# Kernel optimization log

Measured on AMD Instinct MI355X. Metric: run time of the kernel, lower is better.

## Reference

```python
import jax, jax.numpy as jnp
import numpy as np

B, S, DM, DE, H, DH, DC, DCq, DR = 4, 2048, 1024, 1024, 16, 64, 128, 128, 32
SCALE = 1.0 / np.sqrt(DH + DR)


def _rope_tables(seq_len, dim, theta=10000.0):
    inv = 1.0 / (theta ** (jnp.arange(0, dim, 2, dtype=jnp.float32) / dim))  # [dim/2]
    t = jnp.arange(seq_len, dtype=jnp.float32)
    ang = t[:, None] * inv[None, :]  # [S, dim/2]
    return jnp.cos(ang), jnp.sin(ang)


def _apply_rope(xq, xk, cos, sin):
    # xq, xk: [B, S, H, DR]; complex rotary on (even, odd) pairs
    def rot(x):
        s = x.shape
        xr = x.reshape(*s[:-1], s[-1] // 2, 2)
        r, i = xr[..., 0], xr[..., 1]
        c = cos[None, :s[1], None, :]
        sn = sin[None, :s[1], None, :]
        out = jnp.stack([r * c - i * sn, r * sn + i * c], axis=-1)
        return out.reshape(s)
    return rot(xq), rot(xk)


def setup_inputs() -> dict:
    key = jax.random.key(0)
    ks = jax.random.split(key, 10)
    def lin(k, din, dout):
        return 0.02 * jax.random.normal(k, (din, dout), jnp.float32)
    inp = {
        "x": jax.random.normal(ks[0], (B, S, DM), jnp.float32),
        "mask": jnp.tril(jnp.ones((S, S), jnp.float32))[None, None],
        "W_dkv": lin(ks[1], DM, DC),  "b_dkv": jnp.zeros((DC,), jnp.float32),
        "W_dq":  lin(ks[2], DM, DCq), "b_dq":  jnp.zeros((DCq,), jnp.float32),
        "W_uk":  lin(ks[3], DC, DE),  "b_uk":  jnp.zeros((DE,), jnp.float32),
        "W_uv":  lin(ks[4], DC, DE),  "b_uv":  jnp.zeros((DE,), jnp.float32),
        "W_uq":  lin(ks[5], DCq, DE), "b_uq":  jnp.zeros((DE,), jnp.float32),
        "W_qr":  lin(ks[6], DCq, DR * H), "b_qr": jnp.zeros((DR * H,), jnp.float32),
        "W_kr":  lin(ks[7], DM, DR),  "b_kr": jnp.zeros((DR,), jnp.float32),
        "W_o":   lin(ks[8], DE, DM),  "b_o":  jnp.zeros((DM,), jnp.float32),
    }
    return inp


def reference(x, mask, W_dkv, b_dkv, W_dq, b_dq, W_uk, b_uk, W_uv, b_uv,
              W_uq, b_uq, W_qr, b_qr, W_kr, b_kr, W_o, b_o):
    bs, seq_len, _ = x.shape
    cos, sin = _rope_tables(2 * S, DR)

    c_q = x @ W_dq + b_dq            # [B,S,DCq]
    c_kv = x @ W_dkv + b_dkv         # [B,S,DC]
    k_r = x @ W_kr + b_kr            # [B,S,DR]

    q_c = (c_q @ W_uq + b_uq).reshape(bs, seq_len, H, DH)
    k_c = (c_kv @ W_uk + b_uk).reshape(bs, seq_len, H, DH)
    v_c = (c_kv @ W_uv + b_uv).reshape(bs, seq_len, H, DH)

    q_r = (c_q @ W_qr + b_qr).reshape(bs, seq_len, H, DR)
    k_r = jnp.broadcast_to(k_r[:, :, None, :], (bs, seq_len, H, DR))
    q_r, k_r = _apply_rope(q_r, k_r, cos, sin)

    q_t = jnp.concatenate([q_c, q_r], axis=-1)  # [B,S,H,DH+DR]
    k_t = jnp.concatenate([k_c, k_r], axis=-1)

    attn = jnp.einsum('bqhd,bkhd->bhqk', q_t, k_t) * SCALE  # [B,H,S,S]
    m = jnp.where(mask == 0, -jnp.inf, mask)  # faithful masked_fill then add
    attn = attn + m
    p = jax.nn.softmax(attn, axis=-1)
    out = jnp.einsum('bhqk,bkhd->bqhd', p, v_c).reshape(bs, seq_len, H * DH)
    return out @ W_o + b_o
```

## Files before the change

### kernel.cpp

```cpp
#include <hip/hip_runtime.h>
#include <cstdint>
#include <cstddef>

#define S_ 2048
#define B_ 4
#define H_ 16

typedef __attribute__((ext_vector_type(8))) __bf16 bf16x8;
typedef __attribute__((ext_vector_type(4))) __bf16 bf16x4;
typedef __attribute__((ext_vector_type(4))) float f32x4;
typedef __attribute__((ext_vector_type(16))) float f32x16;

__device__ __forceinline__ f32x4 mfma16(bf16x8 a, bf16x8 b, f32x4 c) {
  return __builtin_amdgcn_mfma_f32_16x16x32_bf16(a, b, c, 0, 0, 0);
}
__device__ __forceinline__ f32x16 mfma32(bf16x8 a, bf16x8 b, f32x16 c) {
  return __builtin_amdgcn_mfma_f32_32x32x16_bf16(a, b, c, 0, 0, 0);
}

__device__ __forceinline__ void gll16(const void* g, void* l) {
  __builtin_amdgcn_global_load_lds(
      (__attribute__((address_space(1))) void*)(uintptr_t)g,
      (__attribute__((address_space(3))) void*)(uint32_t)(uintptr_t)l,
      16, 0, 0);
}

__device__ __forceinline__ int cvtpk(float lo, float hi) {
  int r;
  asm("v_cvt_pk_bf16_f32 %0, %1, %2" : "=v"(r) : "v"(lo), "v"(hi));
  return r;
}

union PAU { int w[4]; bf16x8 v; };

__device__ __forceinline__ bf16x8 packPA(int hi, float a0, float a1, float a2,
                                         float a3, float b0, float b1, float b2,
                                         float b3) {
  const int Ylo = cvtpk(a0, a1);
  const int Yhi = cvtpk(a2, a3);
  const int Xlo = cvtpk(b0, b1);
  const int Xhi = cvtpk(b2, b3);
  const int t0 = __shfl_xor(hi ? Ylo : Xlo, 32);
  const int t1 = __shfl_xor(hi ? Yhi : Xhi, 32);
  PAU u;
  u.w[0] = hi ? t0 : Ylo;
  u.w[1] = hi ? t1 : Yhi;
  u.w[2] = hi ? Xlo : t0;
  u.w[3] = hi ? Xhi : t1;
  return u.v;
}


__global__ __launch_bounds__(256) void mla_cvt_x(const float* __restrict__ x,
                                                 __bf16* __restrict__ xb) {
  const size_t i = ((size_t)blockIdx.x * 256 + threadIdx.x) * 8;
  float4 a = *(const float4*)&x[i];
  float4 b = *(const float4*)&x[i + 4];
  bf16x8 v;
  v[0] = (__bf16)a.x; v[1] = (__bf16)a.y; v[2] = (__bf16)a.z; v[3] = (__bf16)a.w;
  v[4] = (__bf16)b.x; v[5] = (__bf16)b.y; v[6] = (__bf16)b.z; v[7] = (__bf16)b.w;
  *(bf16x8*)&xb[i] = v;
}

__global__ void mla_transpose(const float* __restrict__ W, __bf16* __restrict__ WT,
                              int K, int N) {
  __shared__ float tile[32][33];
  const int n0 = blockIdx.x * 32, k0 = blockIdx.y * 32;
  const int tx = threadIdx.x, ty = threadIdx.y;
#pragma unroll
  for (int i = 0; i < 32; i += 8)
    tile[ty + i][tx] = W[(size_t)(k0 + ty + i) * N + n0 + tx];
  __syncthreads();
#pragma unroll
  for (int i = 0; i < 32; i += 8)
    WT[(size_t)(n0 + ty + i) * K + k0 + tx] = (__bf16)tile[tx][ty + i];
}

__global__ void mla_bias(const float* __restrict__ b_dq, const float* __restrict__ b_dkv,
                         const float* __restrict__ b_kr, const float* __restrict__ b_uq,
                         const float* __restrict__ b_qr, const float* __restrict__ b_uk,
                         const float* __restrict__ b_uv, float* __restrict__ bias_d,
                         float* __restrict__ bias_uq, float* __restrict__ bias_ukv) {
  const int t = blockIdx.x * 256 + threadIdx.x;
  if (t < 384)
    bias_d[t] = (t < 128) ? b_dq[t] : (t < 256) ? b_dkv[t - 128]
               : (t < 288) ? b_kr[t - 256] : 0.f;
  if (t < 1536) bias_uq[t] = (t < 1024) ? b_uq[t] : b_qr[t - 1024];
  if (t < 2048) bias_ukv[t] = (t < 1024) ? b_uk[t] : b_uv[t - 1024];
}

__global__ void mla_rope_tab(float* __restrict__ c, float* __restrict__ sn) {
  const int t = blockIdx.x * 256 + threadIdx.x;
  const int s = t >> 4, i = t & 15;
  const float inv = exp2f(-(float)i * (13.287712379549449f / 16.0f));
  const float ang = (float)s * inv;
  c[t] = cosf(ang);
  sn[t] = sinf(ang);
}

template <bool OUTF32>
__global__ __launch_bounds__(256) void gemm_bf16k(
    const __bf16* __restrict__ A, int lda, const __bf16* __restrict__ BT, int ldbt,
    const float* __restrict__ bias, void* __restrict__ Cout, int ldc, int K) {
  const int n0 = blockIdx.x * 128;
  const int m0 = blockIdx.y * 128;
  const int tid = threadIdx.x;
  const int wave = tid >> 6, lane = tid & 63;
  const int g = lane >> 4, li = lane & 15;
  const int wm = (wave >> 1) * 64, wn = (wave & 1) * 64;
  __shared__ __bf16 __attribute__((aligned(16))) ldsA[128 * 32];
  __shared__ __bf16 __attribute__((aligned(16))) ldsB[128 * 32];

  const f32x4 fz = {0.f, 0.f, 0.f, 0.f};
  f32x4 acc[4][4];
#pragma unroll
  for (int i = 0; i < 4; ++i)
#pragma unroll
    for (int j = 0; j < 4; ++j) acc[i][j] = fz;

  const int srow = lane >> 2;
  const int skc = (lane & 3) * 8;

  for (int k0 = 0; k0 < K; k0 += 32) {
    __syncthreads();
#pragma unroll
    for (int c = 0; c < 4; ++c) {
      const int chunk = wave * 4 + c;
      const int r8 = (chunk & 7) * 16 + srow;
      if (chunk < 8)
        gll16(&A[(size_t)(m0 + r8) * lda + k0 + skc], &ldsA[(chunk & 7) * 512]);
      else
        gll16(&BT[(size_t)(n0 + r8) * ldbt + k0 + skc], &ldsB[(chunk & 7) * 512]);
    }
    __syncthreads();

    bf16x8 af[4], bfv[4];
#pragma unroll
    for (int mi = 0; mi < 4; ++mi)
      af[mi] = *(const bf16x8*)&ldsA[(wm + mi * 16 + li) * 32 + g * 8];
#pragma unroll
    for (int ni = 0; ni < 4; ++ni)
      bfv[ni] = *(const bf16x8*)&ldsB[(wn + ni * 16 + li) * 32 + g * 8];
#pragma unroll
    for (int mi = 0; mi < 4; ++mi)
#pragma unroll
      for (int ni = 0; ni < 4; ++ni)
        acc[mi][ni] = mfma16(af[mi], bfv[ni], acc[mi][ni]);
  }

#pragma unroll
  for (int ni = 0; ni < 4; ++ni) {
    const int col = n0 + wn + ni * 16 + li;
    const float bv = bias[col];
#pragma unroll
    for (int mi = 0; mi < 4; ++mi) {
#pragma unroll
      for (int r = 0; r < 4; ++r) {
        const int row = m0 + wm + mi * 16 + 4 * g + r;
        const float v = acc[mi][ni][r] + bv;
        if (OUTF32)
          ((float*)Cout)[(size_t)row * ldc + col] = v;
        else
          ((__bf16*)Cout)[(size_t)row * ldc + col] = (__bf16)v;
      }
    }
  }
}

#define ALPHA_Q 0.14724394f
__global__ __launch_bounds__(256) void mla_build_qk(
    const __bf16* __restrict__ qup, const __bf16* __restrict__ kvup,
    const __bf16* __restrict__ cqkvr, const float* __restrict__ ropec,
    const float* __restrict__ ropes, __bf16* __restrict__ qt,
    __bf16* __restrict__ ktb) {
  const int bs = blockIdx.x;
  const int b = bs >> 11;
  const int s = bs & 2047;
  __shared__ float krr[32];
  if (threadIdx.x < 16) {
    const int i = threadIdx.x;
    const float r = (float)cqkvr[(size_t)bs * 384 + 256 + 2 * i];
    const float im = (float)cqkvr[(size_t)bs * 384 + 256 + 2 * i + 1];
    const float c = ropec[s * 16 + i], sn = ropes[s * 16 + i];
    krr[2 * i] = r * c - im * sn;
    krr[2 * i + 1] = r * sn + im * c;
  }
  __syncthreads();
  for (int idx = threadIdx.x; idx < 1536; idx += 256) {
    const int h = idx / 96, d = idx - h * 96;
    const size_t orow = ((size_t)(b * H_ + h) * S_ + s) * 96;
    float qv, kv;
    if (d < 64) {
      qv = (float)qup[(size_t)bs * 1536 + h * 64 + d];
      kv = (float)kvup[(size_t)bs * 2048 + h * 64 + d];
    } else {
      const int i = (d - 64) >> 1;
      const float c = ropec[s * 16 + i], sn = ropes[s * 16 + i];
      const float r = (float)qup[(size_t)bs * 1536 + 1024 + h * 32 + 2 * i];
      const float im = (float)qup[(size_t)bs * 1536 + 1024 + h * 32 + 2 * i + 1];
      qv = (((d - 64) & 1) == 0) ? (r * c - im * sn) : (r * sn + im * c);
      kv = krr[d - 64];
    }
    qt[orow + d] = (__bf16)(qv * ALPHA_Q);
    ktb[orow + d] = (__bf16)kv;
  }
}

__global__ __launch_bounds__(256) void mla_vtrans(const __bf16* __restrict__ kvup,
                                                  __bf16* __restrict__ vt) {
  const int s0 = blockIdx.x * 64;
  const int bh = blockIdx.y;
  const int b = bh >> 4, h = bh & 15;
  __shared__ __bf16 __attribute__((aligned(16))) tile[64][72];
  const int t = threadIdx.x;
  {
    const int r = t >> 2, c0 = (t & 3) * 16;
    const size_t src = (size_t)(b * S_ + s0 + r) * 2048 + 1024 + h * 64 + c0;
    bf16x8 u0 = *(const bf16x8*)&kvup[src];
    bf16x8 u1 = *(const bf16x8*)&kvup[src + 8];
    *(bf16x8*)&tile[r][c0] = u0;
    *(bf16x8*)&tile[r][c0 + 8] = u1;
  }
  __syncthreads();
  {
    const int d = t >> 2, sc0 = (t & 3) * 16;
    bf16x8 w0, w1;
#pragma unroll
    for (int e = 0; e < 8; ++e) {
      w0[e] = tile[sc0 + e][d];
      w1[e] = tile[sc0 + 8 + e][d];
    }
    const size_t dst = ((size_t)bh * 64 + d) * S_ + s0 + sc0;
    *(bf16x8*)&vt[dst] = w0;
    *(bf16x8*)&vt[dst + 8] = w1;
  }
}

__global__ __launch_bounds__(256, 3) void mla_attn(const __bf16* __restrict__ qt,
                                                   const __bf16* __restrict__ kt,
                                                   const __bf16* __restrict__ vt,
                                                   __bf16* __restrict__ ao) {
  const int qblk = (int)gridDim.x - 1 - blockIdx.x;
  const int bh = blockIdx.y;
  const int wave = threadIdx.x >> 6, lane = threadIdx.x & 63;
  const int hi = lane >> 5, lq = lane & 31;
  const int q0w = qblk * 128 + wave * 32;
  const __bf16* Q = qt + (size_t)bh * S_ * 96;
  const __bf16* Kp = kt + (size_t)bh * S_ * 96;
  const __bf16* Vp = vt + (size_t)bh * 64 * S_;

  __shared__ __bf16 __attribute__((aligned(16))) kbuf[2][12 * 512];
  __shared__ __bf16 __attribute__((aligned(16))) vbuf[2][8 * 512];

  bf16x8 qf[6];
#pragma unroll
  for (int kd = 0; kd < 6; ++kd)
    qf[kd] = *(const bf16x8*)&Q[(size_t)(q0w + lq) * 96 + kd * 16 + hi * 8];

  const f32x16 fz16 = {0.f, 0.f, 0.f, 0.f, 0.f, 0.f, 0.f, 0.f,
                       0.f, 0.f, 0.f, 0.f, 0.f, 0.f, 0.f, 0.f};
  f32x16 o0 = fz16, o1 = fz16;
  float m = -3.0e38f, L = 0.f;

  const int tEnd = (q0w + 31) >> 6;
  const int tMax = qblk * 2 + 1;

  auto stage = [&](int t, int bsel) {
    const int kv0 = t * 64;
#pragma unroll
    for (int i = 0; i < 5; ++i) {
      const int c = wave + 4 * i;
      if (c < 12)
        gll16(&Kp[(size_t)(kv0 + lane) * 96 + c * 8], &kbuf[bsel][c * 512]);
      else
        gll16(&Vp[(size_t)lane * S_ + kv0 + (c - 12) * 8], &vbuf[bsel][(c - 12) * 512]);
    }
  };

  stage(0, 0);
  __syncthreads();

  int bsel = 0;
  for (int t = 0; t <= tMax; ++t) {
    if (t < tMax) stage(t + 1, bsel ^ 1);
    if (t <= tEnd) {
      f32x16 s0 = fz16, s1 = fz16;
#pragma unroll
      for (int kd = 0; kd < 6; ++kd) {
        const int sl = kd * 2 + hi;
        bf16x8 a0 = *(const bf16x8*)&kbuf[bsel][(sl * 64 + lq) * 8];
        bf16x8 a1 = *(const bf16x8*)&kbuf[bsel][(sl * 64 + 32 + lq) * 8];
        s0 = mfma32(a0, qf[kd], s0);
        s1 = mfma32(a1, qf[kd], s1);
      }
      if (t == tEnd) {
        const int qg = q0w + lq;
        const int kvb = t * 64 + 4 * hi;
#pragma unroll
        for (int r = 0; r < 16; ++r) {
          const int crow = (r & 3) + 8 * (r >> 2);
          if (kvb + crow > qg) s0[r] = -3.0e38f;
          if (kvb + 32 + crow > qg) s1[r] = -3.0e38f;
        }
      }
      float tm = s0[0];
#pragma unroll
      for (int r = 1; r < 16; ++r) tm = fmaxf(tm, s0[r]);
#pragma unroll
      for (int r = 0; r < 16; ++r) tm = fmaxf(tm, s1[r]);
      tm = fmaxf(tm, __shfl_xor(tm, 32));
      const float mnew = fmaxf(m, tm);
      float p0[16], p1[16];
      float ps = 0.f;
#pragma unroll
      for (int r = 0; r < 16; ++r) {
        p0[r] = exp2f(s0[r] - mnew);
        p1[r] = exp2f(s1[r] - mnew);
        ps += p0[r] + p1[r];
      }
      ps += __shfl_xor(ps, 32);
      const float sc = exp2f(m - mnew);
      L = L * sc + ps;
      m = mnew;
      o0 *= sc;
      o1 *= sc;
      bf16x8 pa[4];
      pa[0] = packPA(hi, p0[0], p0[1], p0[2], p0[3], p0[4], p0[5], p0[6], p0[7]);
      pa[1] = packPA(hi, p0[8], p0[9], p0[10], p0[11], p0[12], p0[13], p0[14], p0[15]);
      pa[2] = packPA(hi, p1[0], p1[1], p1[2], p1[3], p1[4], p1[5], p1[6], p1[7]);
      pa[3] = packPA(hi, p1[8], p1[9], p1[10], p1[11], p1[12], p1[13], p1[14], p1[15]);
#pragma unroll
      for (int ks = 0; ks < 4; ++ks) {
        const int sl = ks * 2 + hi;
        bf16x8 v0 = *(const bf16x8*)&vbuf[bsel][(sl * 64 + lq) * 8];
        bf16x8 v1 = *(const bf16x8*)&vbuf[bsel][(sl * 64 + 32 + lq) * 8];
        o0 = mfma32(v0, pa[ks], o0);
        o1 = mfma32(v1, pa[ks], o1);
      }
    }
    __syncthreads();
    bsel ^= 1;
  }

  const float invL = 1.0f / L;
  const int bb = bh >> 4, h = bh & 15;
  __bf16* aorow = ao + (size_t)(bb * S_ + q0w + lq) * 1024 + h * 64;
#pragma unroll
  for (int rr = 0; rr < 4; ++rr) {
    bf16x4 w0, w1;
#pragma unroll
    for (int j = 0; j < 4; ++j) {
      w0[j] = (__bf16)(o0[4 * rr + j] * invL);
      w1[j] = (__bf16)(o1[4 * rr + j] * invL);
    }
    *(bf16x4*)&aorow[rr * 8 + 4 * hi] = w0;
    *(bf16x4*)&aorow[32 + rr * 8 + 4 * hi] = w1;
  }
}

extern "C" void kernel_launch(void* const* d_in, const int* in_sizes, int n_in,
                              void* d_out, int out_size, void* d_ws, size_t ws_size,
                              hipStream_t stream) {
  (void)in_sizes; (void)n_in; (void)out_size; (void)ws_size;
  const float* x = (const float*)d_in[0];
  const float* W_dkv = (const float*)d_in[2];
  const float* b_dkv = (const float*)d_in[3];
  const float* W_dq = (const float*)d_in[4];
  const float* b_dq = (const float*)d_in[5];
  const float* W_uk = (const float*)d_in[6];
  const float* b_uk = (const float*)d_in[7];
  const float* W_uv = (const float*)d_in[8];
  const float* b_uv = (const float*)d_in[9];
  const float* W_uq = (const float*)d_in[10];
  const float* b_uq = (const float*)d_in[11];
  const float* W_qr = (const float*)d_in[12];
  const float* b_qr = (const float*)d_in[13];
  const float* W_kr = (const float*)d_in[14];
  const float* b_kr = (const float*)d_in[15];
  const float* W_o = (const float*)d_in[16];
  const float* b_o = (const float*)d_in[17];
  float* out = (float*)d_out;

  char* ws = (char*)d_ws;
  size_t off = 0;
  auto take = [&](size_t nbytes) -> char* {
    char* p = ws + off;
    off += (nbytes + 255) & ~(size_t)255;
    return p;
  };
  __bf16* xb = (__bf16*)take((size_t)8192 * 1024 * 2);
  __bf16* WdT = (__bf16*)take((size_t)384 * 1024 * 2);
  __bf16* WuqT = (__bf16*)take((size_t)1536 * 128 * 2);
  __bf16* WukvT = (__bf16*)take((size_t)2048 * 128 * 2);
  __bf16* WoT = (__bf16*)take((size_t)1024 * 1024 * 2);
  float* bias_d = (float*)take(384 * 4);
  float* bias_uq = (float*)take(1536 * 4);
  float* bias_ukv = (float*)take(2048 * 4);
  float* ropec = (float*)take((size_t)S_ * 16 * 4);
  float* ropes = (float*)take((size_t)S_ * 16 * 4);
  __bf16* cqkvr = (__bf16*)take((size_t)8192 * 384 * 2);
  __bf16* qup = (__bf16*)take((size_t)8192 * 1536 * 2);
  __bf16* kvup = (__bf16*)take((size_t)8192 * 2048 * 2);
  __bf16* qt = (__bf16*)take((size_t)B_ * H_ * S_ * 96 * 2);
  __bf16* ktb = (__bf16*)take((size_t)B_ * H_ * S_ * 96 * 2);
  __bf16* vt = (__bf16*)take((size_t)B_ * H_ * 64 * S_ * 2);
  __bf16* aout = (__bf16*)take((size_t)8192 * 1024 * 2);

  hipMemsetAsync(WdT + (size_t)288 * 1024, 0, (size_t)96 * 1024 * 2, stream);

  mla_cvt_x<<<4096, 256, 0, stream>>>(x, xb);
  mla_transpose<<<dim3(4, 32), dim3(32, 8), 0, stream>>>(W_dq, WdT, 1024, 128);
  mla_transpose<<<dim3(4, 32), dim3(32, 8), 0, stream>>>(W_dkv, WdT + (size_t)128 * 1024, 1024, 128);
  mla_transpose<<<dim3(1, 32), dim3(32, 8), 0, stream>>>(W_kr, WdT + (size_t)256 * 1024, 1024, 32);
  mla_transpose<<<dim3(32, 4), dim3(32, 8), 0, stream>>>(W_uq, WuqT, 128, 1024);
  mla_transpose<<<dim3(16, 4), dim3(32, 8), 0, stream>>>(W_qr, WuqT + (size_t)1024 * 128, 128, 512);
  mla_transpose<<<dim3(32, 4), dim3(32, 8), 0, stream>>>(W_uk, WukvT, 128, 1024);
  mla_transpose<<<dim3(32, 4), dim3(32, 8), 0, stream>>>(W_uv, WukvT + (size_t)1024 * 128, 128, 1024);
  mla_transpose<<<dim3(32, 32), dim3(32, 8), 0, stream>>>(W_o, WoT, 1024, 1024);
  mla_bias<<<8, 256, 0, stream>>>(b_dq, b_dkv, b_kr, b_uq, b_qr, b_uk, b_uv,
                                  bias_d, bias_uq, bias_ukv);
  mla_rope_tab<<<(S_ * 16) / 256, 256, 0, stream>>>(ropec, ropes);

  gemm_bf16k<false><<<dim3(3, 64), 256, 0, stream>>>(xb, 1024, WdT, 1024, bias_d,
                                                     cqkvr, 384, 1024);
  gemm_bf16k<false><<<dim3(12, 64), 256, 0, stream>>>(cqkvr, 384, WuqT, 128, bias_uq,
                                                      qup, 1536, 128);
  gemm_bf16k<false><<<dim3(16, 64), 256, 0, stream>>>(cqkvr + 128, 384, WukvT, 128,
                                                      bias_ukv, kvup, 2048, 128);

  mla_build_qk<<<8192, 256, 0, stream>>>(qup, kvup, cqkvr, ropec, ropes, qt, ktb);
  mla_vtrans<<<dim3(32, 64), 256, 0, stream>>>(kvup, vt);
  mla_attn<<<dim3(16, 64), 256, 0, stream>>>(qt, ktb, vt, aout);

  gemm_bf16k<true><<<dim3(8, 64), 256, 0, stream>>>(aout, 1024, WoT, 1024, b_o, out,
                                                    1024, 1024);
}
```

Baseline: 399.4 us.

## Switch GEMMs to 32x32 MFMA and fuse Q/K scatter into up-projection epilogue

Rewrites the GEMM kernel to use 32x32x16 MFMA with a 64-wide K step and a slice-major LDS layout, replacing the 16x16 tiles. The up-projection GEMMs now write Q (pre-scaled) and K directly into the head-major attention layout in their epilogue. Only the rope parts and V go to smaller intermediate buffers. The old per-token build kernel becomes a small rope-only kernel, which removes a full read and write of the qup/kvup intermediates. The epilogue stores are scattered 2-byte writes with stride 96 elements, which may coalesce poorly.

```diff
diff --git a/kernel.cpp b/kernel.cpp
--- a/kernel.cpp
+++ b/kernel.cpp
@@ -5,15 +5,13 @@
 #define S_ 2048
 #define B_ 4
 #define H_ 16
+#define ALPHA_Q 0.14724394f
 
 typedef __attribute__((ext_vector_type(8))) __bf16 bf16x8;
 typedef __attribute__((ext_vector_type(4))) __bf16 bf16x4;
 typedef __attribute__((ext_vector_type(4))) float f32x4;
 typedef __attribute__((ext_vector_type(16))) float f32x16;
 
-__device__ __forceinline__ f32x4 mfma16(bf16x8 a, bf16x8 b, f32x4 c) {
-  return __builtin_amdgcn_mfma_f32_16x16x32_bf16(a, b, c, 0, 0, 0);
-}
 __device__ __forceinline__ f32x16 mfma32(bf16x8 a, bf16x8 b, f32x16 c) {
   return __builtin_amdgcn_mfma_f32_32x32x16_bf16(a, b, c, 0, 0, 0);
 }
@@ -98,115 +96,118 @@
   sn[t] = sinf(ang);
 }
 
-template <bool OUTF32>
-__global__ __launch_bounds__(256) void gemm_bf16k(
+template <int MODE>
+__global__ __launch_bounds__(256) void gemm32(
     const __bf16* __restrict__ A, int lda, const __bf16* __restrict__ BT, int ldbt,
-    const float* __restrict__ bias, void* __restrict__ Cout, int ldc, int K) {
+    const float* __restrict__ bias, void* __restrict__ C0, void* __restrict__ C1,
+    int ldc, int K) {
   const int n0 = blockIdx.x * 128;
   const int m0 = blockIdx.y * 128;
-  const int tid = threadIdx.x;
-  const int wave = tid >> 6, lane = tid & 63;
-  const int g = lane >> 4, li = lane & 15;
+  const int wave = threadIdx.x >> 6, lane = threadIdx.x & 63;
+  const int hi = lane >> 5, lq = lane & 31;
   const int wm = (wave >> 1) * 64, wn = (wave & 1) * 64;
-  __shared__ __bf16 __attribute__((aligned(16))) ldsA[128 * 32];
-  __shared__ __bf16 __attribute__((aligned(16))) ldsB[128 * 32];
-
-  const f32x4 fz = {0.f, 0.f, 0.f, 0.f};
-  f32x4 acc[4][4];
-#pragma unroll
-  for (int i = 0; i < 4; ++i)
-#pragma unroll
-    for (int j = 0; j < 4; ++j) acc[i][j] = fz;
-
-  const int srow = lane >> 2;
-  const int skc = (lane & 3) * 8;
-
-  for (int k0 = 0; k0 < K; k0 += 32) {
+  __shared__ __bf16 __attribute__((aligned(16))) ldsA[8 * 128 * 8];
+  __shared__ __bf16 __attribute__((aligned(16))) ldsB[8 * 128 * 8];
+
+  const f32x16 fz16 = {0.f, 0.f, 0.f, 0.f, 0.f, 0.f, 0.f, 0.f,
+                       0.f, 0.f, 0.f, 0.f, 0.f, 0.f, 0.f, 0.f};
+  f32x16 acc00 = fz16, acc01 = fz16, acc10 = fz16, acc11 = fz16;
+
+  for (int k0 = 0; k0 < K; k0 += 64) {
     __syncthreads();
 #pragma unroll
-    for (int c = 0; c < 4; ++c) {
-      const int chunk = wave * 4 + c;
-      const int r8 = (chunk & 7) * 16 + srow;
-      if (chunk < 8)
-        gll16(&A[(size_t)(m0 + r8) * lda + k0 + skc], &ldsA[(chunk & 7) * 512]);
-      else
-        gll16(&BT[(size_t)(n0 + r8) * ldbt + k0 + skc], &ldsB[(chunk & 7) * 512]);
+    for (int i = 0; i < 8; ++i) {
+      const int c = wave * 8 + i;
+      if (c < 16) {
+        const int sl = c >> 1, half = c & 1;
+        gll16(&A[(size_t)(m0 + half * 64 + lane) * lda + k0 + sl * 8],
+              &ldsA[(sl * 128 + half * 64) * 8]);
+      } else {
+        const int cc = c - 16;
+        const int sl = cc >> 1, half = cc & 1;
+        gll16(&BT[(size_t)(n0 + half * 64 + lane) * ldbt + k0 + sl * 8],
+              &ldsB[(sl * 128 + half * 64) * 8]);
+      }
     }
     __syncthreads();
 
-    bf16x8 af[4], bfv[4];
-#pragma unroll
-    for (int mi = 0; mi < 4; ++mi)
-      af[mi] = *(const bf16x8*)&ldsA[(wm + mi * 16 + li) * 32 + g * 8];
-#pragma unroll
-    for (int ni = 0; ni < 4; ++ni)
-      bfv[ni] = *(const bf16x8*)&ldsB[(wn + ni * 16 + li) * 32 + g * 8];
-#pragma unroll
-    for (int mi = 0; mi < 4; ++mi)
-#pragma unroll
-      for (int ni = 0; ni < 4; ++ni)
-        acc[mi][ni] = mfma16(af[mi], bfv[ni], acc[mi][ni]);
-  }
-
-#pragma unroll
-  for (int ni = 0; ni < 4; ++ni) {
-    const int col = n0 + wn + ni * 16 + li;
+#pragma unroll
+    for (int ks = 0; ks < 4; ++ks) {
+      const int sl = ks * 2 + hi;
+      bf16x8 a0 = *(const bf16x8*)&ldsA[(sl * 128 + wm + lq) * 8];
+      bf16x8 a1 = *(const bf16x8*)&ldsA[(sl * 128 + wm + 32 + lq) * 8];
+      bf16x8 b0 = *(const bf16x8*)&ldsB[(sl * 128 + wn + lq) * 8];
+      bf16x8 b1 = *(const bf16x8*)&ldsB[(sl * 128 + wn + 32 + lq) * 8];
+      acc00 = mfma32(a0, b0, acc00);
+      acc01 = mfma32(a0, b1, acc01);
+      acc10 = mfma32(a1, b0, acc10);
+      acc11 = mfma32(a1, b1, acc11);
+    }
+  }
+
+  const f32x16* accs[2][2] = {{&acc00, &acc01}, {&acc10, &acc11}};
+#pragma unroll
+  for (int ni = 0; ni < 2; ++ni) {
+    const int col = n0 + wn + ni * 32 + lq;
     const float bv = bias[col];
 #pragma unroll
-    for (int mi = 0; mi < 4; ++mi) {
-#pragma unroll
-      for (int r = 0; r < 4; ++r) {
-        const int row = m0 + wm + mi * 16 + 4 * g + r;
-        const float v = acc[mi][ni][r] + bv;
-        if (OUTF32)
-          ((float*)Cout)[(size_t)row * ldc + col] = v;
-        else
-          ((__bf16*)Cout)[(size_t)row * ldc + col] = (__bf16)v;
-      }
-    }
-  }
-}
-
-#define ALPHA_Q 0.14724394f
-__global__ __launch_bounds__(256) void mla_build_qk(
-    const __bf16* __restrict__ qup, const __bf16* __restrict__ kvup,
-    const __bf16* __restrict__ cqkvr, const float* __restrict__ ropec,
-    const float* __restrict__ ropes, __bf16* __restrict__ qt,
-    __bf16* __restrict__ ktb) {
-  const int bs = blockIdx.x;
-  const int b = bs >> 11;
-  const int s = bs & 2047;
-  __shared__ float krr[32];
-  if (threadIdx.x < 16) {
-    const int i = threadIdx.x;
+    for (int mi = 0; mi < 2; ++mi) {
+      const f32x16& ac = *accs[mi][ni];
+#pragma unroll
+      for (int r = 0; r < 16; ++r) {
+        const int row = m0 + wm + mi * 32 + (r & 3) + 8 * (r >> 2) + 4 * hi;
+        const float v = ac[r] + bv;
+        if (MODE == 0) {
+          ((__bf16*)C0)[(size_t)row * ldc + col] = (__bf16)v;
+        } else if (MODE == 1) {
+          ((float*)C0)[(size_t)row * ldc + col] = v;
+        } else {
+          const int b = row >> 11, s = row & 2047;
+          if (col < 1024) {
+            const int h = col >> 6, d = col & 63;
+            const size_t o = ((size_t)(b * H_ + h) * S_ + s) * 96 + d;
+            if (MODE == 2)
+              ((__bf16*)C0)[o] = (__bf16)(v * ALPHA_Q);
+            else
+              ((__bf16*)C0)[o] = (__bf16)v;
+          } else {
+            if (MODE == 2)
+              ((__bf16*)C1)[(size_t)row * 512 + col - 1024] = (__bf16)v;
+            else
+              ((__bf16*)C1)[(size_t)row * 1024 + col - 1024] = (__bf16)v;
+          }
+        }
+      }
+    }
+  }
+}
+
+__global__ __launch_bounds__(256) void mla_rope_qk(
+    const __bf16* __restrict__ qr, const __bf16* __restrict__ cqkvr,
+    const float* __restrict__ ropec, const float* __restrict__ ropes,
+    __bf16* __restrict__ qt, __bf16* __restrict__ ktb) {
+  const int gid = blockIdx.x * 256 + threadIdx.x;
+  const int bs = gid >> 8;
+  const int h = (gid >> 4) & 15;
+  const int i = gid & 15;
+  const int b = bs >> 11, s = bs & 2047;
+  const float c = ropec[s * 16 + i], sn = ropes[s * 16 + i];
+  const size_t o = ((size_t)(b * H_ + h) * S_ + s) * 96 + 64 + 2 * i;
+  {
+    const float r = (float)qr[(size_t)bs * 512 + h * 32 + 2 * i];
+    const float im = (float)qr[(size_t)bs * 512 + h * 32 + 2 * i + 1];
+    qt[o] = (__bf16)((r * c - im * sn) * ALPHA_Q);
+    qt[o + 1] = (__bf16)((r * sn + im * c) * ALPHA_Q);
+  }
+  {
     const float r = (float)cqkvr[(size_t)bs * 384 + 256 + 2 * i];
     const float im = (float)cqkvr[(size_t)bs * 384 + 256 + 2 * i + 1];
-    const float c = ropec[s * 16 + i], sn = ropes[s * 16 + i];
-    krr[2 * i] = r * c - im * sn;
-    krr[2 * i + 1] = r * sn + im * c;
-  }
-  __syncthreads();
-  for (int idx = threadIdx.x; idx < 1536; idx += 256) {
-    const int h = idx / 96, d = idx - h * 96;
-    const size_t orow = ((size_t)(b * H_ + h) * S_ + s) * 96;
-    float qv, kv;
-    if (d < 64) {
-      qv = (float)qup[(size_t)bs * 1536 + h * 64 + d];
-      kv = (float)kvup[(size_t)bs * 2048 + h * 64 + d];
-    } else {
-      const int i = (d - 64) >> 1;
-      const float c = ropec[s * 16 + i], sn = ropes[s * 16 + i];
-      const float r = (float)qup[(size_t)bs * 1536 + 1024 + h * 32 + 2 * i];
-      const float im = (float)qup[(size_t)bs * 1536 + 1024 + h * 32 + 2 * i + 1];
-      qv = (((d - 64) & 1) == 0) ? (r * c - im * sn) : (r * sn + im * c);
-      kv = krr[d - 64];
-    }
-    qt[orow + d] = (__bf16)(qv * ALPHA_Q);
-    ktb[orow + d] = (__bf16)kv;
-  }
-}
-
-__global__ __launch_bounds__(256) void mla_vtrans(const __bf16* __restrict__ kvup,
+    ktb[o] = (__bf16)(r * c - im * sn);
+    ktb[o + 1] = (__bf16)(r * sn + im * c);
+  }
+}
+
+__global__ __launch_bounds__(256) void mla_vtrans(const __bf16* __restrict__ vv,
                                                   __bf16* __restrict__ vt) {
   const int s0 = blockIdx.x * 64;
   const int bh = blockIdx.y;
@@ -215,9 +216,9 @@
   const int t = threadIdx.x;
   {
     const int r = t >> 2, c0 = (t & 3) * 16;
-    const size_t src = (size_t)(b * S_ + s0 + r) * 2048 + 1024 + h * 64 + c0;
-    bf16x8 u0 = *(const bf16x8*)&kvup[src];
-    bf16x8 u1 = *(const bf16x8*)&kvup[src + 8];
+    const size_t src = (size_t)(b * S_ + s0 + r) * 1024 + h * 64 + c0;
+    bf16x8 u0 = *(const bf16x8*)&vv[src];
+    bf16x8 u1 = *(const bf16x8*)&vv[src + 8];
     *(bf16x8*)&tile[r][c0] = u0;
     *(bf16x8*)&tile[r][c0 + 8] = u1;
   }
@@ -399,8 +400,8 @@
   float* ropec = (float*)take((size_t)S_ * 16 * 4);
   float* ropes = (float*)take((size_t)S_ * 16 * 4);
   __bf16* cqkvr = (__bf16*)take((size_t)8192 * 384 * 2);
-  __bf16* qup = (__bf16*)take((size_t)8192 * 1536 * 2);
-  __bf16* kvup = (__bf16*)take((size_t)8192 * 2048 * 2);
+  __bf16* qr = (__bf16*)take((size_t)8192 * 512 * 2);
+  __bf16* vv = (__bf16*)take((size_t)8192 * 1024 * 2);
   __bf16* qt = (__bf16*)take((size_t)B_ * H_ * S_ * 96 * 2);
   __bf16* ktb = (__bf16*)take((size_t)B_ * H_ * S_ * 96 * 2);
   __bf16* vt = (__bf16*)take((size_t)B_ * H_ * 64 * S_ * 2);
@@ -421,17 +422,17 @@
                                   bias_d, bias_uq, bias_ukv);
   mla_rope_tab<<<(S_ * 16) / 256, 256, 0, stream>>>(ropec, ropes);
 
-  gemm_bf16k<false><<<dim3(3, 64), 256, 0, stream>>>(xb, 1024, WdT, 1024, bias_d,
-                                                     cqkvr, 384, 1024);
-  gemm_bf16k<false><<<dim3(12, 64), 256, 0, stream>>>(cqkvr, 384, WuqT, 128, bias_uq,
-                                                      qup, 1536, 128);
-  gemm_bf16k<false><<<dim3(16, 64), 256, 0, stream>>>(cqkvr + 128, 384, WukvT, 128,
-                                                      bias_ukv, kvup, 2048, 128);
-
-  mla_build_qk<<<8192, 256, 0, stream>>>(qup, kvup, cqkvr, ropec, ropes, qt, ktb);
-  mla_vtrans<<<dim3(32, 64), 256, 0, stream>>>(kvup, vt);
+  gemm32<0><<<dim3(3, 64), 256, 0, stream>>>(xb, 1024, WdT, 1024, bias_d,
+                                             cqkvr, nullptr, 384, 1024);
+  gemm32<2><<<dim3(12, 64), 256, 0, stream>>>(cqkvr, 384, WuqT, 128, bias_uq,
+                                              qt, qr, 0, 128);
+  gemm32<3><<<dim3(16, 64), 256, 0, stream>>>(cqkvr + 128, 384, WukvT, 128,
+                                              bias_ukv, ktb, vv, 0, 128);
+
+  mla_rope_qk<<<8192, 256, 0, stream>>>(qr, cqkvr, ropec, ropes, qt, ktb);
+  mla_vtrans<<<dim3(32, 64), 256, 0, stream>>>(vv, vt);
   mla_attn<<<dim3(16, 64), 256, 0, stream>>>(qt, ktb, vt, aout);
 
-  gemm_bf16k<true><<<dim3(8, 64), 256, 0, stream>>>(aout, 1024, WoT, 1024, b_o, out,
-                                                    1024, 1024);
-}
+  gemm32<1><<<dim3(8, 64), 256, 0, stream>>>(aout, 1024, WoT, 1024, b_o, out,
+                                             nullptr, 1024, 1024);
+}
```

Result: slower. 412.4 us (+3.2%).
